# Optimization experiments

Measured on AMD Instinct MI355X. Metric: run time of the kernel, lower is better.

The kernel has to match this reference:

```python
import jax, jax.numpy as jnp
import numpy as np

NUM_NODES = 15000


def _gcn_conv(x, W, b, src, dst, norm, num_nodes):
    # PyG GCNConv: x' = D^-1/2 (A + I) D^-1/2 (x W) + b
    h = x @ W                                   # [N, out]
    msg = h[src] * norm[:, None]                # gather + scale per edge
    out = jax.ops.segment_sum(msg, dst, num_segments=num_nodes)
    return out + b


def setup_inputs() -> dict:
    key = jax.random.key(0)
    ks = jax.random.split(key, 12)
    T = 100000
    E = 200000
    inp = {
        "x": jax.random.normal(ks[0], (NUM_NODES, 768), jnp.float32),
        "r_emb": jax.random.normal(ks[1], (T, 768), jnp.float32),
        "W1": jax.random.normal(ks[2], (768, 10), jnp.float32) * 0.05,
        "b1": jax.random.normal(ks[3], (10,), jnp.float32) * 0.05,
        "W2": jax.random.normal(ks[4], (10, 128), jnp.float32) * 0.05,
        "b2": jax.random.normal(ks[5], (128,), jnp.float32) * 0.05,
        "W_ih": jax.random.normal(ks[6], (512, 1024), jnp.float32) * 0.03,
        "W_hh": jax.random.normal(ks[7], (512, 128), jnp.float32) * 0.03,
        "b_ih": jax.random.normal(ks[8], (512,), jnp.float32) * 0.03,
        "b_hh": jax.random.normal(ks[9], (512,), jnp.float32) * 0.03,
        "edge_index": jax.random.randint(ks[10], (2, E), 0, NUM_NODES).astype(jnp.int64),
        "triples": jax.random.randint(ks[11], (T, 3), 0, NUM_NODES).astype(jnp.int64),
    }
    return inp


def reference(x, r_emb, W1, b1, W2, b2, W_ih, W_hh, b_ih, b_hh, edge_index, triples):
    N = x.shape[0]
    H = 128  # lstm hidden size
    # --- add self loops, symmetric GCN normalization ---
    loop = jnp.arange(N, dtype=edge_index.dtype)
    src = jnp.concatenate([edge_index[0], loop])
    dst = jnp.concatenate([edge_index[1], loop])
    deg = jax.ops.segment_sum(jnp.ones_like(dst, jnp.float32), dst, num_segments=N)
    dinv = jnp.where(deg > 0, jax.lax.rsqrt(deg), 0.0)
    norm = dinv[src] * dinv[dst]                      # [E+N]
    # --- 2-layer GCN ---
    h = jax.nn.relu(_gcn_conv(x, W1, b1, src, dst, norm, N))   # [N, 10]
    z = _gcn_conv(h, W2, b2, src, dst, norm, N)                # [N, 128]
    # --- per-triple LSTM scoring, batched (seq_len=1, zero init state) ---
    hvec = z[triples[:, 0]]                           # [T, 128]
    tvec = z[triples[:, 2]]                           # [T, 128]
    feat = jnp.concatenate([hvec, r_emb, tvec], axis=-1)       # [T, 1024]
    gates = feat @ W_ih.T + (b_ih + b_hh)             # [T, 512]; h0=0 so W_hh term vanishes
    i_g, f_g, g_g, o_g = jnp.split(gates, 4, axis=-1)  # torch gate order i,f,g,o
    c = jax.nn.sigmoid(i_g) * jnp.tanh(g_g)           # c0 = 0 -> forget term drops
    out = jax.nn.sigmoid(o_g) * jnp.tanh(c)           # [T, 128]
    score = jax.nn.sigmoid(jnp.sum(out, axis=-1))     # [T]
    return score
```

## Files before the change

kernel.cpp:

```cpp
#include <hip/hip_runtime.h>

#define NF 768
#define D1 10
#define D2 128
#define BM 64

typedef __attribute__((ext_vector_type(8))) short bf16x8;
typedef __attribute__((ext_vector_type(16))) float f32x16;

static __device__ __forceinline__ float sigf(float v){ return 1.0f/(1.0f+__expf(-v)); }
static __device__ __forceinline__ float tanhfast(float v){ return 2.0f/(1.0f+__expf(-2.0f*v)) - 1.0f; }
static __device__ __forceinline__ short f2bf(float f){
    unsigned u = __float_as_uint(f);
    u += 0x7fffu + ((u>>16)&1u);
    return (short)(u>>16);
}

static __device__ __forceinline__ void gload16(const void* g, void* l){
    __builtin_amdgcn_global_load_lds(
        (const __attribute__((address_space(1))) unsigned int*)(unsigned long long)g,
        (__attribute__((address_space(3))) unsigned int*)(unsigned long long)l,
        16, 0, 0);
}

static __device__ __forceinline__ bf16x8 cvt8(float4 a, float4 b){
    unsigned u0,u1,u2,u3;
    asm("v_cvt_pk_bf16_f32 %0, %1, %2" : "=v"(u0) : "v"(a.x), "v"(a.y));
    asm("v_cvt_pk_bf16_f32 %0, %1, %2" : "=v"(u1) : "v"(a.z), "v"(a.w));
    asm("v_cvt_pk_bf16_f32 %0, %1, %2" : "=v"(u2) : "v"(b.x), "v"(b.y));
    asm("v_cvt_pk_bf16_f32 %0, %1, %2" : "=v"(u3) : "v"(b.z), "v"(b.w));
    union { unsigned u[4]; bf16x8 v; } r;
    r.u[0]=u0; r.u[1]=u1; r.u[2]=u2; r.u[3]=u3;
    return r.v;
}

__global__ void k_deg(const int* __restrict__ dst, int* __restrict__ cnt, int E){
    int e = blockIdx.x*256 + threadIdx.x;
    if(e<E) atomicAdd(&cnt[dst[e]], 1);
}

__global__ __launch_bounds__(256) void k_scan(const int* __restrict__ cnt,
                                              int* __restrict__ rowptr, int* __restrict__ rowcur,
                                              float* __restrict__ dinv, int N, int E){
    __shared__ int part[256];
    int t = threadIdx.x;
    int C = (N+255)/256;
    int lo = t*C, hi = lo+C; if(hi>N) hi=N; if(lo>N) lo=N;
    int s=0;
    for(int i=lo;i<hi;i++) s += cnt[i];
    part[t]=s;
    __syncthreads();
    if(t==0){
        int run=0;
        for(int i=0;i<256;i++){ int v=part[i]; part[i]=run; run+=v; }
        rowptr[N]=E;
    }
    __syncthreads();
    int run = part[t];
    for(int i=lo;i<hi;i++){
        rowptr[i]=run; rowcur[i]=run; run += cnt[i];
        dinv[i] = rsqrtf((float)cnt[i] + 1.0f);
    }
}

__global__ void k_fill(const int* __restrict__ src, const int* __restrict__ dst,
                       const float* __restrict__ dinv, int* __restrict__ rowcur,
                       int* __restrict__ esrc, float* __restrict__ enorm, int E){
    int e = blockIdx.x*256 + threadIdx.x;
    if(e>=E) return;
    int s=src[e], d=dst[e];
    int pos = atomicAdd(&rowcur[d], 1);
    esrc[pos]=s;
    enorm[pos]=dinv[s]*dinv[d];
}

__global__ __launch_bounds__(256) void k_h1(const float* __restrict__ x,
                                            const float* __restrict__ W1,
                                            float* __restrict__ h1, int N){
    __shared__ float wt[D1*NF];
    for(int idx=threadIdx.x; idx<NF*D1; idx+=256){
        int k=idx/D1, c=idx-k*D1;
        wt[c*NF+k]=W1[idx];
    }
    __syncthreads();
    int row = blockIdx.x*4 + (threadIdx.x>>6);
    int lane = threadIdx.x&63;
    if(row>=N) return;
    const float4* xr = (const float4*)(x + (size_t)row*NF);
    float acc[D1];
#pragma unroll
    for(int c=0;c<D1;c++) acc[c]=0.f;
#pragma unroll
    for(int i=0;i<3;i++){
        float4 v = xr[lane + 64*i];
#pragma unroll
        for(int c=0;c<D1;c++){
            float4 w = *(const float4*)&wt[c*NF + (lane+64*i)*4];
            acc[c] += v.x*w.x + v.y*w.y + v.z*w.z + v.w*w.w;
        }
    }
#pragma unroll
    for(int c=0;c<D1;c++){
        float v=acc[c];
#pragma unroll
        for(int off=32;off;off>>=1) v += __shfl_down(v,off,64);
        acc[c]=v;
    }
    if(lane==0){
#pragma unroll
        for(int c=0;c<D1;c++) h1[(size_t)row*D1+c]=acc[c];
    }
}

__global__ __launch_bounds__(256) void k_gath1(const float* __restrict__ h1,
        const int* __restrict__ rowptr, const int* __restrict__ esrc,
        const float* __restrict__ enorm, const float* __restrict__ dinv,
        const float* __restrict__ b1, float* __restrict__ h, int N){
    int node = blockIdx.x*4 + (threadIdx.x>>6);
    int lane = threadIdx.x&63;
    if(node>=N) return;
    int e0=rowptr[node], e1=rowptr[node+1];
    float acc[D1];
#pragma unroll
    for(int c=0;c<D1;c++) acc[c]=0.f;
    for(int e=e0+lane; e<e1; e+=64){
        int s=esrc[e]; float w=enorm[e];
        const float* hr = h1 + (size_t)s*D1;
#pragma unroll
        for(int c=0;c<D1;c++) acc[c] += hr[c]*w;
    }
    if(lane==0){
        float di=dinv[node], d2=di*di;
        const float* hr = h1 + (size_t)node*D1;
#pragma unroll
        for(int c=0;c<D1;c++) acc[c] += hr[c]*d2;
    }
#pragma unroll
    for(int c=0;c<D1;c++){
        float v=acc[c];
#pragma unroll
        for(int off=32;off;off>>=1) v += __shfl_down(v,off,64);
        acc[c]=v;
    }
    if(lane==0){
#pragma unroll
        for(int c=0;c<D1;c++){
            float v = acc[c] + b1[c];
            h[(size_t)node*D1+c] = v>0.f ? v : 0.f;
        }
    }
}

__global__ __launch_bounds__(128) void k_hz(const float* __restrict__ h,
                                            const float* __restrict__ W2,
                                            float* __restrict__ hz, int N){
    __shared__ float w2s[D1*D2];
    int j = threadIdx.x;
    for(int i=j;i<D1*D2;i+=128) w2s[i]=W2[i];
    __syncthreads();
    int n = blockIdx.x;
    if(n>=N) return;
    const float* hr = h + (size_t)n*D1;
    float acc=0.f;
#pragma unroll
    for(int k=0;k<D1;k++) acc += hr[k]*w2s[k*D2+j];
    hz[(size_t)n*D2+j]=acc;
}

__global__ __launch_bounds__(128) void k_gath2(const float* __restrict__ hz,
        const int* __restrict__ rowptr, const int* __restrict__ esrc,
        const float* __restrict__ enorm, const float* __restrict__ dinv,
        const float* __restrict__ b2, float* __restrict__ zbf, int N){
    int n = blockIdx.x;
    int c = threadIdx.x;
    int e0 = rowptr[n], e1 = rowptr[n+1];
    float di = dinv[n];
    float acc = hz[(size_t)n*D2+c]*di*di + b2[c];
    int e = e0;
    for(; e+1<e1; e+=2){
        int s0=esrc[e], s1=esrc[e+1];
        float w0=enorm[e], w1=enorm[e+1];
        acc += hz[(size_t)s0*D2+c]*w0 + hz[(size_t)s1*D2+c]*w1;
    }
    if(e<e1) acc += hz[(size_t)esrc[e]*D2+c]*enorm[e];
    zbf[(size_t)n*D2+c] = acc;
}

__global__ void k_wimgB(const float* __restrict__ Wih, ushort* __restrict__ img){
    int gid = blockIdx.x*256 + threadIdx.x;
    if(gid >= 12*64*64) return;
    int l = gid & 63;
    int ks16 = (gid>>6) & 63;
    int f = gid >> 12;
    int dd = l & 31, kb = l>>5;
    int wn = f/3, gi = f - wn*3;
    int gbase = (gi==0)?0:((gi==1)?256:384);
    int wrow = gbase + wn*32 + dd;
    int k = ks16*16 + kb*8;
    const float* p = Wih + (size_t)wrow*1024 + k;
    float4 v0=*(const float4*)p, v1=*(const float4*)(p+4);
    bf16x8 o;
    o[0]=f2bf(v0.x); o[1]=f2bf(v0.y); o[2]=f2bf(v0.z); o[3]=f2bf(v0.w);
    o[4]=f2bf(v1.x); o[5]=f2bf(v1.y); o[6]=f2bf(v1.z); o[7]=f2bf(v1.w);
    *(bf16x8*)(img + (size_t)gid*8) = o;
}

__global__ __launch_bounds__(256,2) void k_big(
    const float* __restrict__ remb, const ushort* __restrict__ img,
    const float* __restrict__ zbf, const float* __restrict__ b_ih,
    const float* __restrict__ b_hh, const int* __restrict__ trip,
    float* __restrict__ score, int T)
{
    __shared__ float ring[4][64*64];
    int tid=threadIdx.x, lane=tid&63, w=tid>>6;
    int l31=lane&31, lh=lane>>5;
    int t0=blockIdx.x*BM;

    const int l16 = lane>>4;
    int tc4[4], th4[4], tt4[4], lsl[4];
#pragma unroll
    for(int j=0;j<4;j++){
        int row = w*16 + j*4 + l16;
        int tc = t0 + row; if(tc>=T) tc=T-1;
        tc4[j] = tc;
        th4[j] = trip[3*tc];
        tt4[j] = trip[3*tc+2];
        lsl[j] = ((lane&15) ^ (row&15))*4;
    }

    const ushort* wb0 = img + ((size_t)(w*3+0)*64*64 + lane)*8;
    const ushort* wb1 = img + ((size_t)(w*3+1)*64*64 + lane)*8;
    const ushort* wb2 = img + ((size_t)(w*3+2)*64*64 + lane)*8;
    const int base0 = l31*64;
    const int base1 = (32+l31)*64;
    const int rx = lane&15;

    f32x16 acc[2][3];
    const f32x16 zer = {0,0,0,0,0,0,0,0,0,0,0,0,0,0,0,0};
#pragma unroll
    for(int m=0;m<2;m++)
#pragma unroll
        for(int g=0;g<3;g++) acc[m][g]=zer;

    bf16x8 qb[2][4][3];

#define BISSUE(CN_) if((CN_)<16){ \
    _Pragma("unroll") \
    for(int s_=0;s_<4;s_++){ \
        size_t ko_ = (size_t)((CN_)*4+s_)*512; \
        qb[(CN_)&1][s_][0] = *(const bf16x8*)(wb0+ko_); \
        qb[(CN_)&1][s_][1] = *(const bf16x8*)(wb1+ko_); \
        qb[(CN_)&1][s_][2] = *(const bf16x8*)(wb2+ko_); \
    } }

#define ISSUE(C_) { \
    float* dst_ = &ring[(C_)&3][(w*16)*64]; \
    _Pragma("unroll") \
    for(int j_=0;j_<4;j_++){ \
        const float* src_; \
        if((C_)<2)       src_ = zbf + (size_t)th4[j_]*D2 + (C_)*64 + lsl[j_]; \
        else if((C_)<14) src_ = remb + (size_t)tc4[j_]*NF + ((C_)-2)*64 + lsl[j_]; \
        else             src_ = zbf + (size_t)tt4[j_]*D2 + ((C_)-14)*64 + lsl[j_]; \
        gload16(src_, dst_ + j_*256); \
    } }

#define KSTEP(C_,S_) { \
    const float4 a00_ = *(const float4*)&cur_[base0 + ((((S_)*4+lh*2)  )^rx)*4]; \
    const float4 a01_ = *(const float4*)&cur_[base0 + ((((S_)*4+lh*2)+1)^rx)*4]; \
    bf16x8 A0_ = cvt8(a00_, a01_); \
    const float4 a10_ = *(const float4*)&cur_[base1 + ((((S_)*4+lh*2)  )^rx)*4]; \
    const float4 a11_ = *(const float4*)&cur_[base1 + ((((S_)*4+lh*2)+1)^rx)*4]; \
    bf16x8 A1_ = cvt8(a10_, a11_); \
    acc[0][0]=__builtin_amdgcn_mfma_f32_32x32x16_bf16(A0_,qb[(C_)&1][S_][0],acc[0][0],0,0,0); \
    acc[0][1]=__builtin_amdgcn_mfma_f32_32x32x16_bf16(A0_,qb[(C_)&1][S_][1],acc[0][1],0,0,0); \
    acc[0][2]=__builtin_amdgcn_mfma_f32_32x32x16_bf16(A0_,qb[(C_)&1][S_][2],acc[0][2],0,0,0); \
    acc[1][0]=__builtin_amdgcn_mfma_f32_32x32x16_bf16(A1_,qb[(C_)&1][S_][0],acc[1][0],0,0,0); \
    acc[1][1]=__builtin_amdgcn_mfma_f32_32x32x16_bf16(A1_,qb[(C_)&1][S_][1],acc[1][1],0,0,0); \
    acc[1][2]=__builtin_amdgcn_mfma_f32_32x32x16_bf16(A1_,qb[(C_)&1][S_][2],acc[1][2],0,0,0); \
}

#define CHUNK(C_,W_) { \
    asm volatile("s_waitcnt vmcnt(" W_ ")" ::: "memory"); \
    __builtin_amdgcn_sched_barrier(0); \
    __builtin_amdgcn_s_barrier(); \
    BISSUE((C_)+1) \
    __builtin_amdgcn_sched_barrier(0); \
    if((C_)+3 < 16) { ISSUE((C_)+3) } \
    __builtin_amdgcn_sched_barrier(0); \
    const float* cur_ = &ring[(C_)&3][0]; \
    __builtin_amdgcn_s_setprio(1); \
    KSTEP(C_,0) KSTEP(C_,1) KSTEP(C_,2) KSTEP(C_,3) \
    __builtin_amdgcn_s_setprio(0); \
}

    BISSUE(0)
    __builtin_amdgcn_sched_barrier(0);
    ISSUE(0) ISSUE(1) ISSUE(2)

    CHUNK(0 ,"8")  CHUNK(1 ,"20") CHUNK(2 ,"32") CHUNK(3 ,"32")
    CHUNK(4 ,"32") CHUNK(5 ,"32") CHUNK(6 ,"32") CHUNK(7 ,"32")
    CHUNK(8 ,"32") CHUNK(9 ,"32") CHUNK(10,"32") CHUNK(11,"32")
    CHUNK(12,"32") CHUNK(13,"32") CHUNK(14,"28") CHUNK(15,"24")
#undef CHUNK
#undef KSTEP
#undef ISSUE
#undef BISSUE

    float* rowsum = &ring[0][0];
    __syncthreads();
    if(tid<BM) rowsum[tid]=0.f;
    __syncthreads();
    int d = w*32+l31;
    float bi=b_ih[d]+b_hh[d];
    float bg=b_ih[256+d]+b_hh[256+d];
    float bo=b_ih[384+d]+b_hh[384+d];
#pragma unroll
    for(int m=0;m<2;m++){
#pragma unroll
        for(int r=0;r<16;r++){
            int row = m*32 + (r&3)+8*(r>>2)+4*lh;
            float ig = acc[m][0][r] + bi;
            float gg = acc[m][1][r] + bg;
            float og = acc[m][2][r] + bo;
            float cc = sigf(ig)*tanhfast(gg);
            float ov = sigf(og)*tanhfast(cc);
#pragma unroll
            for(int off=1; off<32; off<<=1) ov += __shfl_xor(ov, off, 64);
            if(l31==0) atomicAdd(&rowsum[row], ov);
        }
    }
    __syncthreads();
    if(tid < BM){
        int t = t0 + tid;
        if(t < T) score[t] = sigf(rowsum[tid]);
    }
}

extern "C" void kernel_launch(void* const* d_in, const int* in_sizes, int n_in,
                              void* d_out, int out_size, void* d_ws, size_t ws_size,
                              hipStream_t stream){
    const float* x    = (const float*)d_in[0];
    const float* remb = (const float*)d_in[1];
    const float* W1   = (const float*)d_in[2];
    const float* b1   = (const float*)d_in[3];
    const float* W2   = (const float*)d_in[4];
    const float* b2   = (const float*)d_in[5];
    const float* Wih  = (const float*)d_in[6];
    const float* b_ih = (const float*)d_in[8];
    const float* b_hh = (const float*)d_in[9];
    const int*   ei   = (const int*)d_in[10];
    const int*   trip = (const int*)d_in[11];
    float* score = (float*)d_out;

    const int N = in_sizes[0]/NF;
    const int E = in_sizes[10]/2;
    const int T = in_sizes[11]/3;
    const int* src = ei;
    const int* dst = ei + E;

    float* ws = (float*)d_ws;
    size_t o = 0;
    ushort* img  = (ushort*)(ws+o); o += (size_t)12*64*64*8/2;
    float* zbf   = ws+o;            o += (size_t)N*D2;
    int*   cnt    = (int*)(ws+o);   o += (size_t)((N+8)&~7);
    int*   rowptr = (int*)(ws+o);   o += (size_t)((N+8)&~7);
    int*   rowcur = (int*)(ws+o);   o += (size_t)((N+8)&~7);
    int*   esrc   = (int*)(ws+o);   o += (size_t)E;
    float* enorm  = ws+o;           o += (size_t)E;
    float* dinv   = ws+o;           o += (size_t)((N+7)&~7);
    float* h1     = ws+o;           o += (size_t)N*D1;
    float* hbuf   = ws+o;           o += (size_t)N*D1;
    float* hz     = ws+o;           o += (size_t)N*D2;
    (void)ws_size; (void)n_in; (void)out_size;

    hipMemsetAsync(cnt, 0, (size_t)N*sizeof(int), stream);

    k_wimgB<<<dim3((12*64*64+255)/256), dim3(256), 0, stream>>>(Wih, img);
    k_deg  <<<dim3((E+255)/256), dim3(256), 0, stream>>>(dst, cnt, E);
    k_scan <<<dim3(1), dim3(256), 0, stream>>>(cnt, rowptr, rowcur, dinv, N, E);
    k_fill <<<dim3((E+255)/256), dim3(256), 0, stream>>>(src, dst, dinv, rowcur, esrc, enorm, E);
    k_h1   <<<dim3((N+3)/4), dim3(256), 0, stream>>>(x, W1, h1, N);
    k_gath1<<<dim3((N+3)/4), dim3(256), 0, stream>>>(h1, rowptr, esrc, enorm, dinv, b1, hbuf, N);
    k_hz   <<<dim3(N), dim3(128), 0, stream>>>(hbuf, W2, hz, N);
    k_gath2<<<dim3(N), dim3(128), 0, stream>>>(hz, rowptr, esrc, enorm, dinv, b2, zbf, N);
    k_big  <<<dim3((T+BM-1)/BM), dim3(256), 0, stream>>>(remb, img, zbf, b_ih, b_hh, trip, score, T);
}
```

Measured before the change: 316.6 us.

## Stage LSTM weight tiles through LDS and halve the K chunk size

```diff
diff --git a/kernel.cpp b/kernel.cpp
--- a/kernel.cpp
+++ b/kernel.cpp
@@ -211,29 +211,22 @@
     const float* __restrict__ b_hh, const int* __restrict__ trip,
     float* __restrict__ score, int T)
 {
-    __shared__ float ring[4][64*64];
+    __shared__ float  Ar[4][64*32];
+    __shared__ ushort Br[2][24*64*8];
     int tid=threadIdx.x, lane=tid&63, w=tid>>6;
     int l31=lane&31, lh=lane>>5;
     int t0=blockIdx.x*BM;
 
-    const int l16 = lane>>4;
-    int tc4[4], th4[4], tt4[4], lsl[4];
-#pragma unroll
-    for(int j=0;j<4;j++){
-        int row = w*16 + j*4 + l16;
-        int tc = t0 + row; if(tc>=T) tc=T-1;
-        tc4[j] = tc;
-        th4[j] = trip[3*tc];
-        tt4[j] = trip[3*tc+2];
-        lsl[j] = ((lane&15) ^ (row&15))*4;
-    }
-
-    const ushort* wb0 = img + ((size_t)(w*3+0)*64*64 + lane)*8;
-    const ushort* wb1 = img + ((size_t)(w*3+1)*64*64 + lane)*8;
-    const ushort* wb2 = img + ((size_t)(w*3+2)*64*64 + lane)*8;
-    const int base0 = l31*64;
-    const int base1 = (32+l31)*64;
-    const int rx = lane&15;
+    const int arow = lane>>3;
+    const int lsl  = ((lane&7) ^ arow)*4;
+    int tcA[2], thA[2], ttA[2];
+#pragma unroll
+    for(int j=0;j<2;j++){
+        int row = w*16 + j*8 + arow;
+        int tc = t0+row; if(tc>=T) tc=T-1;
+        tcA[j]=tc; thA[j]=trip[3*tc]; ttA[j]=trip[3*tc+2];
+    }
+    const int rx = l31&7;
 
     f32x16 acc[2][3];
     const f32x16 zer = {0,0,0,0,0,0,0,0,0,0,0,0,0,0,0,0};
@@ -242,71 +235,74 @@
 #pragma unroll
         for(int g=0;g<3;g++) acc[m][g]=zer;
 
-    bf16x8 qb[2][4][3];
-
-#define BISSUE(CN_) if((CN_)<16){ \
+#define AISSUE(C_) if((C_)<32){ \
     _Pragma("unroll") \
-    for(int s_=0;s_<4;s_++){ \
-        size_t ko_ = (size_t)((CN_)*4+s_)*512; \
-        qb[(CN_)&1][s_][0] = *(const bf16x8*)(wb0+ko_); \
-        qb[(CN_)&1][s_][1] = *(const bf16x8*)(wb1+ko_); \
-        qb[(CN_)&1][s_][2] = *(const bf16x8*)(wb2+ko_); \
+    for(int j_=0;j_<2;j_++){ \
+        const float* s_; \
+        if((C_)<4)       s_ = zbf + (size_t)thA[j_]*D2 + (C_)*32 + lsl; \
+        else if((C_)<28) s_ = remb + (size_t)tcA[j_]*NF + ((C_)-4)*32 + lsl; \
+        else             s_ = zbf + (size_t)ttA[j_]*D2 + ((C_)-28)*32 + lsl; \
+        gload16(s_, &Ar[(C_)&3][(w*16 + j_*8)*32]); \
     } }
 
-#define ISSUE(C_) { \
-    float* dst_ = &ring[(C_)&3][(w*16)*64]; \
+#define BISSUE(C_) if((C_)<32){ \
     _Pragma("unroll") \
-    for(int j_=0;j_<4;j_++){ \
-        const float* src_; \
-        if((C_)<2)       src_ = zbf + (size_t)th4[j_]*D2 + (C_)*64 + lsl[j_]; \
-        else if((C_)<14) src_ = remb + (size_t)tc4[j_]*NF + ((C_)-2)*64 + lsl[j_]; \
-        else             src_ = zbf + (size_t)tt4[j_]*D2 + ((C_)-14)*64 + lsl[j_]; \
-        gload16(src_, dst_ + j_*256); \
+    for(int j_=0;j_<6;j_++){ \
+        const int i_ = w*6+j_, f_ = i_>>1, s_ = i_&1; \
+        gload16(img + ((size_t)(f_*64 + (C_)*2 + s_)*64 + lane)*8, \
+                &Br[(C_)&1][(f_*2+s_)*64*8]); \
     } }
 
 #define KSTEP(C_,S_) { \
-    const float4 a00_ = *(const float4*)&cur_[base0 + ((((S_)*4+lh*2)  )^rx)*4]; \
-    const float4 a01_ = *(const float4*)&cur_[base0 + ((((S_)*4+lh*2)+1)^rx)*4]; \
-    bf16x8 A0_ = cvt8(a00_, a01_); \
-    const float4 a10_ = *(const float4*)&cur_[base1 + ((((S_)*4+lh*2)  )^rx)*4]; \
-    const float4 a11_ = *(const float4*)&cur_[base1 + ((((S_)*4+lh*2)+1)^rx)*4]; \
-    bf16x8 A1_ = cvt8(a10_, a11_); \
-    acc[0][0]=__builtin_amdgcn_mfma_f32_32x32x16_bf16(A0_,qb[(C_)&1][S_][0],acc[0][0],0,0,0); \
-    acc[0][1]=__builtin_amdgcn_mfma_f32_32x32x16_bf16(A0_,qb[(C_)&1][S_][1],acc[0][1],0,0,0); \
-    acc[0][2]=__builtin_amdgcn_mfma_f32_32x32x16_bf16(A0_,qb[(C_)&1][S_][2],acc[0][2],0,0,0); \
-    acc[1][0]=__builtin_amdgcn_mfma_f32_32x32x16_bf16(A1_,qb[(C_)&1][S_][0],acc[1][0],0,0,0); \
-    acc[1][1]=__builtin_amdgcn_mfma_f32_32x32x16_bf16(A1_,qb[(C_)&1][S_][1],acc[1][1],0,0,0); \
-    acc[1][2]=__builtin_amdgcn_mfma_f32_32x32x16_bf16(A1_,qb[(C_)&1][S_][2],acc[1][2],0,0,0); \
+    const float* ar_ = &Ar[(C_)&3][0]; \
+    const ushort* br_ = &Br[(C_)&1][0]; \
+    const int q0_ = (S_)*4 + lh*2; \
+    float4 a00_ = *(const float4*)&ar_[ l31*32      + ((q0_  )^rx)*4 ]; \
+    float4 a01_ = *(const float4*)&ar_[ l31*32      + ((q0_+1)^rx)*4 ]; \
+    bf16x8 A0_ = cvt8(a00_,a01_); \
+    float4 a10_ = *(const float4*)&ar_[ (32+l31)*32 + ((q0_  )^rx)*4 ]; \
+    float4 a11_ = *(const float4*)&ar_[ (32+l31)*32 + ((q0_+1)^rx)*4 ]; \
+    bf16x8 A1_ = cvt8(a10_,a11_); \
+    bf16x8 B0_ = *(const bf16x8*)&br_[(((w*3+0)*2+(S_))*64 + lane)*8]; \
+    bf16x8 B1_ = *(const bf16x8*)&br_[(((w*3+1)*2+(S_))*64 + lane)*8]; \
+    bf16x8 B2_ = *(const bf16x8*)&br_[(((w*3+2)*2+(S_))*64 + lane)*8]; \
+    acc[0][0]=__builtin_amdgcn_mfma_f32_32x32x16_bf16(A0_,B0_,acc[0][0],0,0,0); \
+    acc[0][1]=__builtin_amdgcn_mfma_f32_32x32x16_bf16(A0_,B1_,acc[0][1],0,0,0); \
+    acc[0][2]=__builtin_amdgcn_mfma_f32_32x32x16_bf16(A0_,B2_,acc[0][2],0,0,0); \
+    acc[1][0]=__builtin_amdgcn_mfma_f32_32x32x16_bf16(A1_,B0_,acc[1][0],0,0,0); \
+    acc[1][1]=__builtin_amdgcn_mfma_f32_32x32x16_bf16(A1_,B1_,acc[1][1],0,0,0); \
+    acc[1][2]=__builtin_amdgcn_mfma_f32_32x32x16_bf16(A1_,B2_,acc[1][2],0,0,0); \
 }
 
 #define CHUNK(C_,W_) { \
     asm volatile("s_waitcnt vmcnt(" W_ ")" ::: "memory"); \
+    __builtin_amdgcn_s_barrier(); \
     __builtin_amdgcn_sched_barrier(0); \
-    __builtin_amdgcn_s_barrier(); \
     BISSUE((C_)+1) \
+    AISSUE((C_)+3) \
     __builtin_amdgcn_sched_barrier(0); \
-    if((C_)+3 < 16) { ISSUE((C_)+3) } \
-    __builtin_amdgcn_sched_barrier(0); \
-    const float* cur_ = &ring[(C_)&3][0]; \
     __builtin_amdgcn_s_setprio(1); \
-    KSTEP(C_,0) KSTEP(C_,1) KSTEP(C_,2) KSTEP(C_,3) \
+    KSTEP(C_,0) KSTEP(C_,1) \
     __builtin_amdgcn_s_setprio(0); \
 }
 
-    BISSUE(0)
+    AISSUE(0) AISSUE(1) BISSUE(0) AISSUE(2)
     __builtin_amdgcn_sched_barrier(0);
-    ISSUE(0) ISSUE(1) ISSUE(2)
-
-    CHUNK(0 ,"8")  CHUNK(1 ,"20") CHUNK(2 ,"32") CHUNK(3 ,"32")
-    CHUNK(4 ,"32") CHUNK(5 ,"32") CHUNK(6 ,"32") CHUNK(7 ,"32")
-    CHUNK(8 ,"32") CHUNK(9 ,"32") CHUNK(10,"32") CHUNK(11,"32")
-    CHUNK(12,"32") CHUNK(13,"32") CHUNK(14,"28") CHUNK(15,"24")
+
+    CHUNK(0 ,"2") CHUNK(1 ,"2") CHUNK(2 ,"2") CHUNK(3 ,"2")
+    CHUNK(4 ,"2") CHUNK(5 ,"2") CHUNK(6 ,"2") CHUNK(7 ,"2")
+    CHUNK(8 ,"2") CHUNK(9 ,"2") CHUNK(10,"2") CHUNK(11,"2")
+    CHUNK(12,"2") CHUNK(13,"2") CHUNK(14,"2") CHUNK(15,"2")
+    CHUNK(16,"2") CHUNK(17,"2") CHUNK(18,"2") CHUNK(19,"2")
+    CHUNK(20,"2") CHUNK(21,"2") CHUNK(22,"2") CHUNK(23,"2")
+    CHUNK(24,"2") CHUNK(25,"2") CHUNK(26,"2") CHUNK(27,"2")
+    CHUNK(28,"2") CHUNK(29,"2") CHUNK(30,"0") CHUNK(31,"0")
 #undef CHUNK
 #undef KSTEP
-#undef ISSUE
 #undef BISSUE
-
-    float* rowsum = &ring[0][0];
+#undef AISSUE
+
+    float* rowsum = &Ar[0][0];
     __syncthreads();
     if(tid<BM) rowsum[tid]=0.f;
     __syncthreads();
```

New measurement: 324.5 us. 2.5% more time.
